# Kernel tuning notes

Hardware: AMD Instinct MI355X
Metric: run time of the kernel (lower is better)

Reference implementation:

```python
import jax, jax.numpy as jnp
import numpy as np

B, S, I, H = 64, 256, 1024, 1024


def setup_inputs() -> dict:
    key = jax.random.key(0)
    stdv = 1.0 / np.sqrt(H)
    inp = {}
    key, kx = jax.random.split(key)
    inp["x"] = jax.random.normal(kx, (B, S, I), jnp.float32)
    names = ["W_f", "Wm_f", "W_i", "Wm_i", "W_o", "Wm_o", "W_c", "Wm_c",
             "U_f", "Um_f", "U_i", "Um_i", "U_o", "Um_o", "U_c", "Um_c",
             "b_f", "b_i", "b_o", "b_c"]
    for n in names:
        key, sub = jax.random.split(key)
        if n.startswith("W"):
            shape = (H, I)
        elif n.startswith("U"):
            shape = (H, H)
        else:
            shape = (H,)
        inp[n] = jax.random.uniform(sub, shape, jnp.float32, -stdv, stdv)
    return inp


def _mlin(x, W, Wm):
    # MaskedLinear, wise='feat': sigmoid(x @ Wm^T) * (x @ W^T)
    return jax.nn.sigmoid(x @ Wm.T) * (x @ W.T)


def reference(x, W_f, Wm_f, W_i, Wm_i, W_o, Wm_o, W_c, Wm_c,
              U_f, Um_f, U_i, Um_i, U_o, Um_o, U_c, Um_c,
              b_f, b_i, b_o, b_c):
    # input-side masked linears depend only on x: hoist out of the recurrence
    xf = jnp.moveaxis(_mlin(x, W_f, Wm_f), 1, 0)  # (S,B,H)
    xi = jnp.moveaxis(_mlin(x, W_i, Wm_i), 1, 0)
    xo = jnp.moveaxis(_mlin(x, W_o, Wm_o), 1, 0)
    xc = jnp.moveaxis(_mlin(x, W_c, Wm_c), 1, 0)

    def step(carry, g):
        h, c = carry
        gf, gi, go, gc = g
        f = jax.nn.sigmoid(gf + _mlin(h, U_f, Um_f) + b_f)
        i = jax.nn.sigmoid(gi + _mlin(h, U_i, Um_i) + b_i)
        o = jax.nn.sigmoid(go + _mlin(h, U_o, Um_o) + b_o)
        c = jnp.tanh(gc + _mlin(h, U_c, Um_c) + b_c) * i + f * c
        h = o * c
        return (h, c), h

    h0 = jnp.zeros((B, H), x.dtype)
    (h, c), out = jax.lax.scan(step, (h0, h0), (xf, xi, xo, xc))
    output = jnp.moveaxis(out, 0, 1)  # (B,S,H)
    return output, h[None], c[None]  # h,c: (1,B,H)
```

## Files before the change

### kernel.cpp

```cpp
#include <hip/hip_runtime.h>

typedef float f32x4 __attribute__((ext_vector_type(4)));
typedef _Float16 f16x8 __attribute__((ext_vector_type(8)));
typedef _Float16 f16x4 __attribute__((ext_vector_type(4)));
typedef unsigned int u32x2 __attribute__((ext_vector_type(2)));

typedef const __attribute__((address_space(1))) unsigned int* gptr_t;
typedef __attribute__((address_space(3))) unsigned int* lptr_t;

__device__ __forceinline__ unsigned short f2h_u(float f){
  union { _Float16 h; unsigned short u; } cv; cv.h = (_Float16)f; return cv.u;
}
__device__ __forceinline__ float h2f(unsigned short u){
  union { unsigned short u; _Float16 h; } cv; cv.u = u; return (float)cv.h;
}
__device__ __forceinline__ float sigmoidf_(float x){ return 1.0f / (1.0f + __expf(-x)); }
__device__ __forceinline__ unsigned umax_(unsigned a, unsigned b){ return a > b ? a : b; }

#define ISSUEC(LO, HI, c)                                                      \
  _Pragma("unroll")                                                            \
  for (int i = 0; i < 8; ++i){                                                 \
    const int p0 = pbase + (c) * 16 + (i & 1) * 8;                             \
    const int ro = ((i >> 1) * 16 + r) * 4;                                    \
    const unsigned short* alo_ = hb2 + (size_t)p0 * 256 + ro;                  \
    const unsigned short* ahi_ = hb2 + (size_t)(p0 + 1) * 256 + ro;            \
    asm volatile("global_load_dwordx2 %0, %1, off sc0 sc1"                     \
                 : "=v"(LO[i]) : "v"(alo_) : "memory");                        \
    asm volatile("global_load_dwordx2 %0, %1, off sc0 sc1"                     \
                 : "=v"(HI[i]) : "v"(ahi_) : "memory");                        \
  }

#define WAITVALC(LO, HI, c)                                                    \
  for (;;){                                                                    \
    asm volatile("s_waitcnt vmcnt(0)" ::: "memory");                           \
    __builtin_amdgcn_sched_barrier(0);                                         \
    unsigned mx_ = 0;                                                          \
    _Pragma("unroll")                                                          \
    for (int i = 0; i < 8; ++i)                                                \
      mx_ = umax_(mx_, umax_(umax_(LO[i][0], LO[i][1]),                        \
                             umax_(HI[i][0], HI[i][1])));                      \
    if (__all(mx_ != 0xFFFFFFFFu)) break;                                      \
    ISSUEC(LO, HI, c);                                                         \
  }

#define COMPC2(LO, HI, c)                                                      \
  _Pragma("unroll")                                                            \
  for (int kk = 0; kk < 2; ++kk)                                               \
    _Pragma("unroll")                                                          \
    for (int nt = 0; nt < 2; ++nt)                                             \
      _Pragma("unroll")                                                        \
      for (int mt = 0; mt < 4; ++mt){                                          \
        const int i_ = mt * 2 + kk;                                            \
        f16x8 hf_ = __builtin_shufflevector(*(const f16x4*)&LO[i_],            \
                                            *(const f16x4*)&HI[i_],            \
                                            0, 1, 2, 3, 4, 5, 6, 7);           \
        acc[nt][mt] = __builtin_amdgcn_mfma_f32_16x16x32_f16(                  \
            uf[nt][(c) * 2 + kk], hf_, acc[nt][mt], 0, 0, 0);                  \
      }

__global__ __launch_bounds__(256) void cvt_x(const float* __restrict__ in,
                                             unsigned short* __restrict__ out){
  int idx = blockIdx.x * 256 + threadIdx.x;
  int d4 = idx * 4;
  int s = d4 >> 16, b = (d4 >> 10) & 63, k = d4 & 1023;
  const float4 v = *(const float4*)(in + (size_t)b * 262144 + (size_t)s * 1024 + k);
  ushort4 o;
  o.x = f2h_u(v.x); o.y = f2h_u(v.y); o.z = f2h_u(v.z); o.w = f2h_u(v.w);
  *(ushort4*)(out + d4) = o;
}

struct P8 { const float* p[8]; };

__global__ __launch_bounds__(256) void cvt_w8(P8 mats, unsigned short* __restrict__ out){
  int idx = blockIdx.x * 256 + threadIdx.x;
  int e = idx * 4;
  int mi = e >> 20, off = e & 1048575;
  const float4 v = *(const float4*)(mats.p[mi] + off);
  ushort4 o;
  o.x = f2h_u(v.x); o.y = f2h_u(v.y); o.z = f2h_u(v.z); o.w = f2h_u(v.w);
  *(ushort4*)(out + e) = o;
}

__global__ __launch_bounds__(256) void pack8(P8 mats, unsigned short* __restrict__ out){
  int idx = blockIdx.x * 256 + threadIdx.x;
  int e = idx * 4;
  int j = e >> 10, k = e & 1023;
  int m = j & 7, row = j >> 3;
  const float4 v = *(const float4*)(mats.p[m] + (size_t)row * 1024 + k);
  ushort4 o;
  o.x = f2h_u(v.x); o.y = f2h_u(v.y); o.z = f2h_u(v.z); o.w = f2h_u(v.w);
  *(ushort4*)(out + e) = o;
}

__global__ __launch_bounds__(256, 2) void gemmz(
    const unsigned short* __restrict__ Xh,
    const unsigned short* __restrict__ Wg,
    unsigned short* __restrict__ Z01,
    unsigned short* __restrict__ Z23){
  __shared__ unsigned short As[128 * 32];
  __shared__ unsigned short Bl[128 * 32];
  __shared__ unsigned short Bm[128 * 32];
  const int tid = threadIdx.x;
  const int wave = tid >> 6, lane = tid & 63;
  const int r = lane & 15, q = lane >> 4;
  const int bid0 = blockIdx.x;
  const int bid = (bid0 & 7) * 512 + (bid0 >> 3);
  const int m0 = (bid & 127) * 128;
  const int n0 = ((bid >> 7) & 7) * 128;
  const int g  = bid >> 10;
  const int wm = wave >> 1, wn = wave & 1;

  const unsigned short* WL = Wg + ((size_t)(2 * g) << 20);
  const unsigned short* WM = WL + (1u << 20);

  f32x4 accL[4][4], accM[4][4];
#pragma unroll
  for (int a = 0; a < 4; ++a)
#pragma unroll
    for (int b = 0; b < 4; ++b){ accL[a][b] = 0.f; accM[a][b] = 0.f; }

  const int st_rl = lane >> 2;
  const int st_s0 = lane & 3;

  for (int kt = 0; kt < 32; ++kt){
    const int k0 = kt * 32;
#pragma unroll
    for (int j = 0; j < 2; ++j){
      const int c = wave * 2 + j;
      const int row = c * 16 + st_rl;
      const int slot = st_s0 ^ ((row >> 1) & 3);
      const unsigned short* sA = Xh + (size_t)(m0 + row) * 1024 + k0 + slot * 8;
      const unsigned short* sL = WL + (size_t)(n0 + row) * 1024 + k0 + slot * 8;
      const unsigned short* sM = WM + (size_t)(n0 + row) * 1024 + k0 + slot * 8;
      __builtin_amdgcn_global_load_lds((gptr_t)sA, (lptr_t)(As + c * 512), 16, 0, 0);
      __builtin_amdgcn_global_load_lds((gptr_t)sL, (lptr_t)(Bl + c * 512), 16, 0, 0);
      __builtin_amdgcn_global_load_lds((gptr_t)sM, (lptr_t)(Bm + c * 512), 16, 0, 0);
    }
    __syncthreads();

    f16x8 af[4], bl[4], bm[4];
#pragma unroll
    for (int mt = 0; mt < 4; ++mt){
      const int row = wm * 64 + mt * 16 + r;
      const int slot = q ^ ((row >> 1) & 3);
      af[mt] = *(const f16x8*)(As + row * 32 + slot * 8);
    }
#pragma unroll
    for (int nt = 0; nt < 4; ++nt){
      const int row = wn * 64 + nt * 16 + r;
      const int slot = q ^ ((row >> 1) & 3);
      bl[nt] = *(const f16x8*)(Bl + row * 32 + slot * 8);
      bm[nt] = *(const f16x8*)(Bm + row * 32 + slot * 8);
    }
#pragma unroll
    for (int nt = 0; nt < 4; ++nt)
#pragma unroll
      for (int mt = 0; mt < 4; ++mt){
        accL[mt][nt] = __builtin_amdgcn_mfma_f32_16x16x32_f16(af[mt], bl[nt], accL[mt][nt], 0, 0, 0);
        accM[mt][nt] = __builtin_amdgcn_mfma_f32_16x16x32_f16(af[mt], bm[nt], accM[mt][nt], 0, 0, 0);
      }
    __syncthreads();
  }

  unsigned short* Zp = (g < 2) ? (Z01 + ((size_t)g << 24)) : (Z23 + ((size_t)(g - 2) << 24));
#pragma unroll
  for (int mt = 0; mt < 4; ++mt)
#pragma unroll
    for (int nt = 0; nt < 4; ++nt){
      f32x4 aL = accL[mt][nt], aM = accM[mt][nt];
      union { ushort4 u; uint2 d; } o;
      o.u.x = f2h_u(aL[0] * sigmoidf_(aM[0]));
      o.u.y = f2h_u(aL[1] * sigmoidf_(aM[1]));
      o.u.z = f2h_u(aL[2] * sigmoidf_(aM[2]));
      o.u.w = f2h_u(aL[3] * sigmoidf_(aM[3]));
      const int gn = n0 + wn * 64 + nt * 16 + r;
      const int gm = m0 + wm * 64 + mt * 16 + q * 4;
      *(uint2*)(Zp + (size_t)gn * 16384 + gm) = o.d;
    }
}

__global__ __launch_bounds__(256, 1) void lstm_rec(
    const unsigned short* __restrict__ zF, const unsigned short* __restrict__ zI,
    const unsigned short* __restrict__ zO, const unsigned short* __restrict__ zC,
    const unsigned short* __restrict__ Ug,
    const float* __restrict__ bF, const float* __restrict__ bI,
    const float* __restrict__ bO, const float* __restrict__ bC,
    unsigned short* __restrict__ hh2,
    float* __restrict__ out){
  const int tid = threadIdx.x, wave = tid >> 6, lane = tid & 63;
  const int bi = blockIdx.x, n0 = bi * 4, j0 = bi * 32;
  const int r = lane & 15, q = lane >> 4;
  const int pbase = wave * 64 + 2 * q;
  __shared__ __align__(16) float part[2][4][64][36];

  f16x8 uf[2][8];
#pragma unroll
  for (int nt = 0; nt < 2; ++nt)
#pragma unroll
    for (int kk = 0; kk < 8; ++kk)
      uf[nt][kk] = *(const f16x8*)(Ug + (size_t)(j0 + nt * 16 + r) * 1024 + wave * 256 + kk * 32 + q * 8);

  const int cb = tid >> 2, cl = tid & 3;
  const float bFv = bF[n0 + cl], bIv = bI[n0 + cl], bOv = bO[n0 + cl], bCv = bC[n0 + cl];
  const size_t zb = (size_t)(n0 + cl) * 16384 + cb;
  float c_reg = 0.f;

#pragma unroll 1
  for (int s = 0; s < 256; ++s){
    float zf = h2f(zF[zb + s * 64]);
    float zi = h2f(zI[zb + s * 64]);
    float zo = h2f(zO[zb + s * 64]);
    float zc = h2f(zC[zb + s * 64]);

    f32x4 acc[2][4];
#pragma unroll
    for (int nt = 0; nt < 2; ++nt)
#pragma unroll
      for (int mt = 0; mt < 4; ++mt) acc[nt][mt] = 0.f;

    if (s > 0){
      const unsigned short* hb2 = hh2 + (size_t)(s - 1) * 65536;
      u32x2 Alo[8], Ahi[8], Blo[8], Bhi[8];
      ISSUEC(Alo, Ahi, 0);
      WAITVALC(Alo, Ahi, 0);
      ISSUEC(Blo, Bhi, 1);
      COMPC2(Alo, Ahi, 0);
      WAITVALC(Blo, Bhi, 1);
      ISSUEC(Alo, Ahi, 2);
      COMPC2(Blo, Bhi, 1);
      WAITVALC(Alo, Ahi, 2);
      ISSUEC(Blo, Bhi, 3);
      COMPC2(Alo, Ahi, 2);
      WAITVALC(Blo, Bhi, 3);
      COMPC2(Blo, Bhi, 3);
    }

    const int pp = s & 1;
#pragma unroll
    for (int nt = 0; nt < 2; ++nt)
#pragma unroll
      for (int mt = 0; mt < 4; ++mt)
        *(f32x4*)&part[pp][wave][mt * 16 + r][nt * 16 + q * 4] = acc[nt][mt];
    __syncthreads();

    f32x4 y0 = 0.f, y1 = 0.f;
#pragma unroll
    for (int w = 0; w < 4; ++w){
      y0 += *(const f32x4*)&part[pp][w][cb][cl * 8];
      y1 += *(const f32x4*)&part[pp][w][cb][cl * 8 + 4];
    }

    float fg = sigmoidf_(zf + y0[0] * sigmoidf_(y0[1]) + bFv);
    float ig = sigmoidf_(zi + y0[2] * sigmoidf_(y0[3]) + bIv);
    float og = sigmoidf_(zo + y1[0] * sigmoidf_(y1[1]) + bOv);
    float cg = tanhf   (zc + y1[2] * sigmoidf_(y1[3]) + bCv);
    c_reg = cg * ig + fg * c_reg;
    float h = og * c_reg;

    float hn = __shfl_xor(h, 1);
    if (!(cl & 1)){
      unsigned int pv = (unsigned)f2h_u(h) | ((unsigned)f2h_u(hn) << 16);
      const unsigned short* hw = hh2 + (size_t)s * 65536 + bi * 256 + cb * 4 + cl;
      asm volatile("global_store_dword %0, %1, off sc0 sc1" :: "v"(hw), "v"(pv) : "memory");
    }
    if (s == 255){
      out[16777216 + cb * 1024 + n0 + cl] = h;
      out[16777216 + 65536 + cb * 1024 + n0 + cl] = c_reg;
    }
  }
}

__global__ __launch_bounds__(256) void expand_out(const unsigned short* __restrict__ hh2,
                                                  float* __restrict__ out){
  int idx = blockIdx.x * 256 + threadIdx.x;
  int p = idx & 255, s = (idx >> 8) & 255, cb = idx >> 16;
  f16x4 v = *(const f16x4*)(hh2 + (size_t)s * 65536 + p * 256 + cb * 4);
  float4 f = { (float)v[0], (float)v[1], (float)v[2], (float)v[3] };
  *(float4*)(out + ((size_t)cb * 256 + s) * 1024 + p * 4) = f;
}

extern "C" void kernel_launch(void* const* d_in, const int* in_sizes, int n_in,
                              void* d_out, int out_size, void* d_ws, size_t ws_size,
                              hipStream_t stream){
  (void)in_sizes; (void)n_in; (void)out_size; (void)ws_size;
  char* ws = (char*)d_ws;
  const float* bF = (const float*)d_in[17];
  const float* bI = (const float*)d_in[18];
  const float* bO = (const float*)d_in[19];
  const float* bC = (const float*)d_in[20];
  float* outp = (float*)d_out;
  P8 w8, u8;
  for (int m = 0; m < 8; ++m){
    w8.p[m] = (const float*)d_in[1 + m];
    u8.p[m] = (const float*)d_in[9 + m];
  }

  unsigned short* xh  = (unsigned short*)(ws);
  unsigned short* wg  = (unsigned short*)(ws + 33554432);
  unsigned short* ug  = (unsigned short*)(ws + 50331648);
  unsigned short* z23 = (unsigned short*)(ws + 67108864);
  unsigned short* hh2 = (unsigned short*)(ws + 134217728);
  unsigned short* z01 = (unsigned short*)d_out;

  (void)hipMemsetAsync(hh2, 0xFF, 33554432, stream);
  cvt_x<<<16384, 256, 0, stream>>>((const float*)d_in[0], xh);
  cvt_w8<<<8192, 256, 0, stream>>>(w8, wg);
  pack8<<<8192, 256, 0, stream>>>(u8, ug);
  gemmz<<<4096, 256, 0, stream>>>(xh, wg, z01, z23);

  const unsigned short* zF = z01;
  const unsigned short* zI = z01 + 16777216;
  const unsigned short* zO = z23;
  const unsigned short* zC = z23 + 16777216;

  void* args[] = { (void*)&zF, (void*)&zI, (void*)&zO, (void*)&zC, (void*)&ug,
                   (void*)&bF, (void*)&bI, (void*)&bO, (void*)&bC,
                   (void*)&hh2, (void*)&outp };
  if (hipLaunchCooperativeKernel((const void*)lstm_rec, dim3(256), dim3(256), args, 0u, stream) != hipSuccess)
    lstm_rec<<<256, 256, 0, stream>>>(zF, zI, zO, zC, ug, bF, bI, bO, bC, hh2, outp);

  expand_out<<<16384, 256, 0, stream>>>(hh2, outp);
}
```

Before: 1.455 ms.

## Restructure LSTM recurrence to 128 blocks of 512 threads with 16-byte h exchange

```diff
diff --git a/kernel.cpp b/kernel.cpp
--- a/kernel.cpp
+++ b/kernel.cpp
@@ -3,7 +3,7 @@
 typedef float f32x4 __attribute__((ext_vector_type(4)));
 typedef _Float16 f16x8 __attribute__((ext_vector_type(8)));
 typedef _Float16 f16x4 __attribute__((ext_vector_type(4)));
-typedef unsigned int u32x2 __attribute__((ext_vector_type(2)));
+typedef unsigned int u32x4 __attribute__((ext_vector_type(4)));
 
 typedef const __attribute__((address_space(1))) unsigned int* gptr_t;
 typedef __attribute__((address_space(3))) unsigned int* lptr_t;
@@ -17,46 +17,37 @@
 __device__ __forceinline__ float sigmoidf_(float x){ return 1.0f / (1.0f + __expf(-x)); }
 __device__ __forceinline__ unsigned umax_(unsigned a, unsigned b){ return a > b ? a : b; }
 
-#define ISSUEC(LO, HI, c)                                                      \
+#define GP(w,b,sp) ((((w)*64 + (b))<<6) + ((sp)<<2))
+
+#define ISSUE16(DST, c)                                                        \
   _Pragma("unroll")                                                            \
-  for (int i = 0; i < 8; ++i){                                                 \
-    const int p0 = pbase + (c) * 16 + (i & 1) * 8;                             \
-    const int ro = ((i >> 1) * 16 + r) * 4;                                    \
-    const unsigned short* alo_ = hb2 + (size_t)p0 * 256 + ro;                  \
-    const unsigned short* ahi_ = hb2 + (size_t)(p0 + 1) * 256 + ro;            \
-    asm volatile("global_load_dwordx2 %0, %1, off sc0 sc1"                     \
-                 : "=v"(LO[i]) : "v"(alo_) : "memory");                        \
-    asm volatile("global_load_dwordx2 %0, %1, off sc0 sc1"                     \
-                 : "=v"(HI[i]) : "v"(ahi_) : "memory");                        \
-  }
-
-#define WAITVALC(LO, HI, c)                                                    \
+  for (int mt = 0; mt < 4; ++mt){                                              \
+    const unsigned short* a_ = hb2 +                                           \
+        (size_t)(pb + (c) * 4) * 512 + (size_t)(mt * 16 + r) * 8;              \
+    asm volatile("global_load_dwordx4 %0, %1, off sc0 sc1"                     \
+                 : "=v"(DST[mt]) : "v"(a_) : "memory");                        \
+  }
+
+#define WAITVAL16(DST, c)                                                      \
   for (;;){                                                                    \
     asm volatile("s_waitcnt vmcnt(0)" ::: "memory");                           \
     __builtin_amdgcn_sched_barrier(0);                                         \
     unsigned mx_ = 0;                                                          \
     _Pragma("unroll")                                                          \
-    for (int i = 0; i < 8; ++i)                                                \
-      mx_ = umax_(mx_, umax_(umax_(LO[i][0], LO[i][1]),                        \
-                             umax_(HI[i][0], HI[i][1])));                      \
+    for (int mt = 0; mt < 4; ++mt)                                             \
+      mx_ = umax_(mx_, umax_(umax_(DST[mt][0], DST[mt][1]),                    \
+                             umax_(DST[mt][2], DST[mt][3])));                  \
     if (__all(mx_ != 0xFFFFFFFFu)) break;                                      \
-    ISSUEC(LO, HI, c);                                                         \
-  }
-
-#define COMPC2(LO, HI, c)                                                      \
+    ISSUE16(DST, c);                                                           \
+  }
+
+#define COMP16(DST, c)                                                         \
   _Pragma("unroll")                                                            \
-  for (int kk = 0; kk < 2; ++kk)                                               \
+  for (int nt = 0; nt < 4; ++nt)                                               \
     _Pragma("unroll")                                                          \
-    for (int nt = 0; nt < 2; ++nt)                                             \
-      _Pragma("unroll")                                                        \
-      for (int mt = 0; mt < 4; ++mt){                                          \
-        const int i_ = mt * 2 + kk;                                            \
-        f16x8 hf_ = __builtin_shufflevector(*(const f16x4*)&LO[i_],            \
-                                            *(const f16x4*)&HI[i_],            \
-                                            0, 1, 2, 3, 4, 5, 6, 7);           \
-        acc[nt][mt] = __builtin_amdgcn_mfma_f32_16x16x32_f16(                  \
-            uf[nt][(c) * 2 + kk], hf_, acc[nt][mt], 0, 0, 0);                  \
-      }
+    for (int mt = 0; mt < 4; ++mt)                                             \
+      acc[nt][mt] = __builtin_amdgcn_mfma_f32_16x16x32_f16(                    \
+          uf[nt][(c)], *(const f16x8*)&DST[mt], acc[nt][mt], 0, 0, 0);
 
 __global__ __launch_bounds__(256) void cvt_x(const float* __restrict__ in,
                                              unsigned short* __restrict__ out){
@@ -179,28 +170,29 @@
     }
 }
 
-__global__ __launch_bounds__(256, 1) void lstm_rec(
+__global__ __launch_bounds__(512, 1) void lstm_rec(
     const unsigned short* __restrict__ zF, const unsigned short* __restrict__ zI,
     const unsigned short* __restrict__ zO, const unsigned short* __restrict__ zC,
     const unsigned short* __restrict__ Ug,
     const float* __restrict__ bF, const float* __restrict__ bI,
     const float* __restrict__ bO, const float* __restrict__ bC,
-    unsigned short* __restrict__ hh2,
+    unsigned short* __restrict__ hh3,
     float* __restrict__ out){
   const int tid = threadIdx.x, wave = tid >> 6, lane = tid & 63;
-  const int bi = blockIdx.x, n0 = bi * 4, j0 = bi * 32;
+  const int bi = blockIdx.x, n0 = bi * 8, j0 = bi * 64;
   const int r = lane & 15, q = lane >> 4;
-  const int pbase = wave * 64 + 2 * q;
-  __shared__ __align__(16) float part[2][4][64][36];
-
-  f16x8 uf[2][8];
-#pragma unroll
-  for (int nt = 0; nt < 2; ++nt)
-#pragma unroll
-    for (int kk = 0; kk < 8; ++kk)
-      uf[nt][kk] = *(const f16x8*)(Ug + (size_t)(j0 + nt * 16 + r) * 1024 + wave * 256 + kk * 32 + q * 8);
-
-  const int cb = tid >> 2, cl = tid & 3;
+  const int pb = 16 * wave + q;
+  extern __shared__ float part[];
+
+  f16x8 uf[4][4];
+#pragma unroll
+  for (int nt = 0; nt < 4; ++nt)
+#pragma unroll
+    for (int c = 0; c < 4; ++c)
+      uf[nt][c] = *(const f16x8*)(Ug + (size_t)(j0 + nt * 16 + r) * 1024 +
+                                  wave * 128 + c * 32 + q * 8);
+
+  const int cb = tid >> 3, cl = tid & 7;
   const float bFv = bF[n0 + cl], bIv = bI[n0 + cl], bOv = bO[n0 + cl], bCv = bC[n0 + cl];
   const size_t zb = (size_t)(n0 + cl) * 16384 + cb;
   float c_reg = 0.f;
@@ -212,43 +204,43 @@
     float zo = h2f(zO[zb + s * 64]);
     float zc = h2f(zC[zb + s * 64]);
 
-    f32x4 acc[2][4];
-#pragma unroll
-    for (int nt = 0; nt < 2; ++nt)
+    f32x4 acc[4][4];
+#pragma unroll
+    for (int nt = 0; nt < 4; ++nt)
 #pragma unroll
       for (int mt = 0; mt < 4; ++mt) acc[nt][mt] = 0.f;
 
     if (s > 0){
-      const unsigned short* hb2 = hh2 + (size_t)(s - 1) * 65536;
-      u32x2 Alo[8], Ahi[8], Blo[8], Bhi[8];
-      ISSUEC(Alo, Ahi, 0);
-      WAITVALC(Alo, Ahi, 0);
-      ISSUEC(Blo, Bhi, 1);
-      COMPC2(Alo, Ahi, 0);
-      WAITVALC(Blo, Bhi, 1);
-      ISSUEC(Alo, Ahi, 2);
-      COMPC2(Blo, Bhi, 1);
-      WAITVALC(Alo, Ahi, 2);
-      ISSUEC(Blo, Bhi, 3);
-      COMPC2(Alo, Ahi, 2);
-      WAITVALC(Blo, Bhi, 3);
-      COMPC2(Blo, Bhi, 3);
-    }
-
-    const int pp = s & 1;
-#pragma unroll
-    for (int nt = 0; nt < 2; ++nt)
+      const unsigned short* hb2 = hh3 + (size_t)(s - 1) * 65536;
+      u32x4 hA[4], hB[4];
+      ISSUE16(hA, 0);
+      WAITVAL16(hA, 0);
+      ISSUE16(hB, 1);
+      COMP16(hA, 0);
+      WAITVAL16(hB, 1);
+      ISSUE16(hA, 2);
+      COMP16(hB, 1);
+      WAITVAL16(hA, 2);
+      ISSUE16(hB, 3);
+      COMP16(hA, 2);
+      WAITVAL16(hB, 3);
+      COMP16(hB, 3);
+    }
+
+#pragma unroll
+    for (int nt = 0; nt < 4; ++nt)
 #pragma unroll
       for (int mt = 0; mt < 4; ++mt)
-        *(f32x4*)&part[pp][wave][mt * 16 + r][nt * 16 + q * 4] = acc[nt][mt];
+        *(f32x4*)&part[wave * 4352 + (mt * 16 + r) * 68 + nt * 16 + q * 4] = acc[nt][mt];
     __syncthreads();
 
     f32x4 y0 = 0.f, y1 = 0.f;
 #pragma unroll
-    for (int w = 0; w < 4; ++w){
-      y0 += *(const f32x4*)&part[pp][w][cb][cl * 8];
-      y1 += *(const f32x4*)&part[pp][w][cb][cl * 8 + 4];
-    }
+    for (int w = 0; w < 8; ++w){
+      y0 += *(const f32x4*)&part[w * 4352 + cb * 68 + cl * 8];
+      y1 += *(const f32x4*)&part[w * 4352 + cb * 68 + cl * 8 + 4];
+    }
+    __syncthreads();
 
     float fg = sigmoidf_(zf + y0[0] * sigmoidf_(y0[1]) + bFv);
     float ig = sigmoidf_(zi + y0[2] * sigmoidf_(y0[3]) + bIv);
@@ -257,11 +249,17 @@
     c_reg = cg * ig + fg * c_reg;
     float h = og * c_reg;
 
-    float hn = __shfl_xor(h, 1);
-    if (!(cl & 1)){
-      unsigned int pv = (unsigned)f2h_u(h) | ((unsigned)f2h_u(hn) << 16);
-      const unsigned short* hw = hh2 + (size_t)s * 65536 + bi * 256 + cb * 4 + cl;
-      asm volatile("global_store_dword %0, %1, off sc0 sc1" :: "v"(hw), "v"(pv) : "memory");
+    float h1 = __shfl_down(h, 1), h2v = __shfl_down(h, 2), h3 = __shfl_down(h, 3),
+          h4 = __shfl_down(h, 4), h5 = __shfl_down(h, 5), h6 = __shfl_down(h, 6),
+          h7 = __shfl_down(h, 7);
+    if (cl == 0){
+      u32x4 pv;
+      pv[0] = (unsigned)f2h_u(h)   | ((unsigned)f2h_u(h1) << 16);
+      pv[1] = (unsigned)f2h_u(h2v) | ((unsigned)f2h_u(h3) << 16);
+      pv[2] = (unsigned)f2h_u(h4)  | ((unsigned)f2h_u(h5) << 16);
+      pv[3] = (unsigned)f2h_u(h6)  | ((unsigned)f2h_u(h7) << 16);
+      const unsigned short* hw = hh3 + (size_t)s * 65536 + (size_t)bi * 512 + cb * 8;
+      asm volatile("global_store_dwordx4 %0, %1, off sc0 sc1" :: "v"(hw), "v"(pv) : "memory");
     }
     if (s == 255){
       out[16777216 + cb * 1024 + n0 + cl] = h;
@@ -270,13 +268,19 @@
   }
 }
 
-__global__ __launch_bounds__(256) void expand_out(const unsigned short* __restrict__ hh2,
+__global__ __launch_bounds__(256) void expand_out(const unsigned short* __restrict__ hh3,
                                                   float* __restrict__ out){
   int idx = blockIdx.x * 256 + threadIdx.x;
-  int p = idx & 255, s = (idx >> 8) & 255, cb = idx >> 16;
-  f16x4 v = *(const f16x4*)(hh2 + (size_t)s * 65536 + p * 256 + cb * 4);
-  float4 f = { (float)v[0], (float)v[1], (float)v[2], (float)v[3] };
-  *(float4*)(out + ((size_t)cb * 256 + s) * 1024 + p * 4) = f;
+  int s = idx >> 13, rem = idx & 8191;
+  int p = rem >> 6, cb = rem & 63;
+  const unsigned short* src = hh3 + (size_t)idx * 8;
+  ushort4 a = *(const ushort4*)src;
+  ushort4 c = *(const ushort4*)(src + 4);
+  size_t o = ((size_t)cb * 256 + s) * 1024 + p * 8;
+  float4 f0 = { h2f(a.x), h2f(a.y), h2f(a.z), h2f(a.w) };
+  float4 f1 = { h2f(c.x), h2f(c.y), h2f(c.z), h2f(c.w) };
+  *(float4*)(out + o) = f0;
+  *(float4*)(out + o + 4) = f1;
 }
 
 extern "C" void kernel_launch(void* const* d_in, const int* in_sizes, int n_in,
@@ -299,10 +303,10 @@
   unsigned short* wg  = (unsigned short*)(ws + 33554432);
   unsigned short* ug  = (unsigned short*)(ws + 50331648);
   unsigned short* z23 = (unsigned short*)(ws + 67108864);
-  unsigned short* hh2 = (unsigned short*)(ws + 134217728);
+  unsigned short* hh3 = (unsigned short*)(ws + 134217728);
   unsigned short* z01 = (unsigned short*)d_out;
 
-  (void)hipMemsetAsync(hh2, 0xFF, 33554432, stream);
+  (void)hipMemsetAsync(hh3, 0xFF, 33554432, stream);
   cvt_x<<<16384, 256, 0, stream>>>((const float*)d_in[0], xh);
   cvt_w8<<<8192, 256, 0, stream>>>(w8, wg);
   pack8<<<8192, 256, 0, stream>>>(u8, ug);
@@ -315,9 +319,11 @@
 
   void* args[] = { (void*)&zF, (void*)&zI, (void*)&zO, (void*)&zC, (void*)&ug,
                    (void*)&bF, (void*)&bI, (void*)&bO, (void*)&bC,
-                   (void*)&hh2, (void*)&outp };
-  if (hipLaunchCooperativeKernel((const void*)lstm_rec, dim3(256), dim3(256), args, 0u, stream) != hipSuccess)
-    lstm_rec<<<256, 256, 0, stream>>>(zF, zI, zO, zC, ug, bF, bI, bO, bC, hh2, outp);
-
-  expand_out<<<16384, 256, 0, stream>>>(hh2, outp);
-}
+                   (void*)&hh3, (void*)&outp };
+  size_t shmem = 8 * 64 * 68 * sizeof(float);
+  if (hipLaunchCooperativeKernel((const void*)lstm_rec, dim3(128), dim3(512),
+                                 args, (unsigned)shmem, stream) != hipSuccess)
+    lstm_rec<<<128, 512, shmem, stream>>>(zF, zI, zO, zC, ug, bF, bI, bO, bC, hh3, outp);
+
+  expand_out<<<8192, 256, 0, stream>>>(hh3, outp);
+}
```

After: 2.161 ms. 48.6% more time.
